# Kernel optimization log

Measured on AMD Instinct MI355X. Metric: run time of the kernel, lower is better.

The kernel has to match this reference:

```python
import jax, jax.numpy as jnp
import numpy as np

BS, S, D, H, DFF, L = 8, 1024, 256, 8, 1024, 3
DK = D // H
NEG = -1e32


def setup_inputs() -> dict:
    key = jax.random.key(0)
    ks = jax.random.split(key, 10)
    r = lambda k, shp: jax.random.normal(k, shp, jnp.float32) * 0.02
    return {
        "q_embed_data": jax.random.normal(ks[0], (BS, S, D), jnp.float32),
        "qa_embed_data": jax.random.normal(ks[1], (BS, S, D), jnp.float32),
        "Wk": r(ks[2], (L, D, D)), "bk": jnp.zeros((L, D), jnp.float32),
        "Wv": r(ks[3], (L, D, D)), "bv": jnp.zeros((L, D), jnp.float32),
        "Wo": r(ks[4], (L, D, D)), "bo": jnp.zeros((L, D), jnp.float32),
        "gammas": r(ks[5], (L, H)),
        "ln1_g": jnp.ones((L, D), jnp.float32), "ln1_b": jnp.zeros((L, D), jnp.float32),
        "W1": r(ks[6], (L, D, DFF)), "b1": jnp.zeros((L, DFF), jnp.float32),
        "W2": r(ks[7], (L, DFF, D)), "b2": jnp.zeros((L, D), jnp.float32),
        "ln2_g": jnp.ones((L, D), jnp.float32), "ln2_b": jnp.zeros((L, D), jnp.float32),
    }


def _layernorm(x, g, b, eps=1e-5):
    mu = x.mean(-1, keepdims=True)
    var = ((x - mu) ** 2).mean(-1, keepdims=True)
    return (x - mu) * jax.lax.rsqrt(var + eps) * g + b


def _attn(xq, xk, xv, Wk, bk, Wv, bv, Wo, bo, gamma, mask, zero_pad):
    # kq_same=1: q and k both use k_linear
    bs = xq.shape[0]
    q = (xq @ Wk + bk).reshape(bs, S, H, DK).transpose(0, 2, 1, 3)  # bhsd
    k = (xk @ Wk + bk).reshape(bs, S, H, DK).transpose(0, 2, 1, 3)
    v = (xv @ Wv + bv).reshape(bs, S, H, DK).transpose(0, 2, 1, 3)
    scores = jnp.einsum('bhid,bhjd->bhij', q, k) / np.float32(np.sqrt(DK))
    mf = mask.astype(scores.dtype)
    # no-grad decay branch (detached in torch)
    p = jax.nn.softmax(jnp.where(mask, scores, NEG), axis=-1) * mf
    distcum = jnp.cumsum(p, axis=-1)
    disttot = p.sum(axis=-1, keepdims=True)
    idx = jnp.arange(S)
    pos = jnp.abs(idx[None, :] - idx[:, None]).astype(jnp.float32)[None, None]
    dist = jnp.sqrt(jnp.clip((disttot - distcum) * pos, 0.0, None))
    dist = jax.lax.stop_gradient(dist)
    g = -jax.nn.softplus(gamma)[None, :, None, None]  # (1,H,1,1)
    total_effect = jnp.clip(jnp.exp(dist * g), 1e-5, 1e5)
    scores = scores * total_effect
    attn = jax.nn.softmax(jnp.where(mask, scores, NEG), axis=-1)
    if zero_pad:
        attn = attn.at[:, :, 0, :].set(0.0)
    out = jnp.einsum('bhij,bhjd->bhid', attn, v)
    out = out.transpose(0, 2, 1, 3).reshape(bs, S, D)
    return out @ Wo + bo


def _block(i, xq, xk, xv, mask, zero_pad, apply_pos, P):
    Wk, bk, Wv, bv, Wo, bo, gam, l1g, l1b, W1, b1, W2, b2, l2g, l2b = [p[i] for p in P]
    q2 = _attn(xq, xk, xv, Wk, bk, Wv, bv, Wo, bo, gam, mask, zero_pad)
    x = _layernorm(xq + q2, l1g, l1b)
    if apply_pos:
        ff = jax.nn.relu(x @ W1 + b1) @ W2 + b2
        x = _layernorm(x + ff, l2g, l2b)
    return x


def _forward(q_embed_data, qa_embed_data, Wk, bk, Wv, bv, Wo, bo, gammas,
             ln1_g, ln1_b, W1, b1, W2, b2, ln2_g, ln2_b):
    P = (Wk, bk, Wv, bv, Wo, bo, gammas, ln1_g, ln1_b, W1, b1, W2, b2, ln2_g, ln2_b)
    tri_incl = jnp.tril(jnp.ones((S, S), bool))[None, None]       # mask=1: peek current+past
    tri_excl = jnp.tril(jnp.ones((S, S), bool), -1)[None, None]   # mask=0: strictly past
    x, y = q_embed_data, qa_embed_data
    # blocks_1 (n_blocks=1): mask=1, apply_pos=True, self-attn on y
    y = _block(0, y, y, y, tri_incl, False, True, P)
    # blocks_2 (2*n_blocks=2): alternate (mask=1, no FFN) / (mask=0, zero_pad, FFN, values=y)
    x = _block(1, x, x, x, tri_incl, False, False, P)
    x = _block(2, x, x, y, tri_excl, True, True, P)
    return x


def reference(q_embed_data, qa_embed_data, Wk, bk, Wv, bv, Wo, bo, gammas,
              ln1_g, ln1_b, W1, b1, W2, b2, ln2_g, ln2_b):
    return _forward(q_embed_data, qa_embed_data, Wk, bk, Wv, bv, Wo, bo, gammas,
                    ln1_g, ln1_b, W1, b1, W2, b2, ln2_g, ln2_b)
```

## Files before the change

kernel.cpp:

```cpp
#include <hip/hip_runtime.h>

typedef unsigned short u16;
typedef float f32x4 __attribute__((ext_vector_type(4)));
typedef __bf16 bf16x8 __attribute__((ext_vector_type(8)));
typedef u16 u16x8 __attribute__((ext_vector_type(8)));
typedef u16 u16x4 __attribute__((ext_vector_type(4)));

__device__ __forceinline__ u16 f2bf(float f) {
  union { float f; unsigned u; } v; v.f = f;
  unsigned r = (v.u + 0x7FFFu + ((v.u >> 16) & 1u)) >> 16;
  return (u16)r;
}
__device__ __forceinline__ unsigned cvtpk_bf16(float lo, float hi) {
  unsigned r;
  asm("v_cvt_pk_bf16_f32 %0, %1, %2" : "=v"(r) : "v"(lo), "v"(hi));
  return r;
}
__device__ __forceinline__ float wred_sum(float v) {
#pragma unroll
  for (int o = 32; o >= 1; o >>= 1) v += __shfl_xor(v, o);
  return v;
}

template <int RELU, int WF32, int WBF, int WVT>
__global__ __launch_bounds__(256) void gemm_kernel(
    const u16* __restrict__ A, const u16* __restrict__ Bt,
    const float* __restrict__ bias, float* __restrict__ C,
    u16* __restrict__ Cbf, int M, int N, int K) {
  __shared__ u16 As[64 * 64];
  __shared__ u16 Bs[64 * 64];
  const int tid = threadIdx.x;
  const int lane = tid & 63;
  const int w = tid >> 6;
  const int m0 = blockIdx.x * 64;
  const int n0 = blockIdx.y * 64;
  const int wr = (w >> 1) * 32;
  const int wc = (w & 1) * 32;
  const int l15 = lane & 15, hi = lane >> 4;

  f32x4 acc[2][2] = {};

  for (int k0 = 0; k0 < K; k0 += 64) {
#pragma unroll
    for (int rep = 0; rep < 2; ++rep) {
      int idx = tid + rep * 256;
      int row = idx >> 3, c8 = idx & 7;
      int cs = ((c8 ^ (row & 7)) << 3);
      __builtin_amdgcn_global_load_lds(
          (const __attribute__((address_space(1))) void*)(A + (size_t)(m0 + row) * K + k0 + cs),
          (__attribute__((address_space(3))) void*)(&As[idx * 8]), 16, 0, 0);
      __builtin_amdgcn_global_load_lds(
          (const __attribute__((address_space(1))) void*)(Bt + (size_t)(n0 + row) * K + k0 + cs),
          (__attribute__((address_space(3))) void*)(&Bs[idx * 8]), 16, 0, 0);
    }
    __syncthreads();
#pragma unroll
    for (int kk = 0; kk < 2; ++kk) {
      int kb = (kk * 32 + (hi << 3)) << 1;
      bf16x8 af[2], bfr[2];
#pragma unroll
      for (int mf = 0; mf < 2; ++mf) {
        int m = wr + mf * 16 + l15;
        af[mf] = *(const bf16x8*)((const char*)As + m * 128 + (kb ^ ((m & 7) << 4)));
      }
#pragma unroll
      for (int nf = 0; nf < 2; ++nf) {
        int n = wc + nf * 16 + l15;
        bfr[nf] = *(const bf16x8*)((const char*)Bs + n * 128 + (kb ^ ((n & 7) << 4)));
      }
#pragma unroll
      for (int mf = 0; mf < 2; ++mf)
#pragma unroll
        for (int nf = 0; nf < 2; ++nf)
          acc[mf][nf] = __builtin_amdgcn_mfma_f32_16x16x32_bf16(af[mf], bfr[nf], acc[mf][nf], 0, 0, 0);
    }
    __syncthreads();
  }

#pragma unroll
  for (int mf = 0; mf < 2; ++mf)
#pragma unroll
    for (int nf = 0; nf < 2; ++nf) {
      int col = n0 + wc + nf * 16 + l15;
      float bia = bias[col];
      u16x4 tv;
#pragma unroll
      for (int r = 0; r < 4; ++r) {
        int row = m0 + wr + mf * 16 + (hi << 2) + r;
        float val = acc[mf][nf][r] + bia;
        if (RELU) val = fmaxf(val, 0.f);
        if (WF32) C[(size_t)row * N + col] = val;
        if (WBF) Cbf[(size_t)row * N + col] = f2bf(val);
        if (WVT) tv[r] = f2bf(val);
      }
      if (WVT) {
        int row0 = m0 + wr + mf * 16 + (hi << 2);
        size_t addr = (((size_t)(row0 >> 10) * 8 + (col >> 5)) * 32 + (col & 31)) * 1024 + (row0 & 1023);
        *(u16x4*)(Cbf + addr) = tv;
      }
    }
}

__global__ __launch_bounds__(256) void gemm_kv_kernel(
    const u16* __restrict__ A, const u16* __restrict__ Bt,
    const float* __restrict__ biasK, const float* __restrict__ biasV,
    u16* __restrict__ qkbf, u16* __restrict__ vT, int M, int N, int K) {
  __shared__ u16 As[64 * 64];
  __shared__ u16 Bs[64 * 64];
  const int tid = threadIdx.x;
  const int lane = tid & 63;
  const int w = tid >> 6;
  const int m0 = blockIdx.x * 64;
  const int n0 = blockIdx.y * 64;
  const int wr = (w >> 1) * 32;
  const int wc = (w & 1) * 32;
  const int l15 = lane & 15, hi = lane >> 4;

  f32x4 acc[2][2] = {};

  for (int k0 = 0; k0 < K; k0 += 64) {
#pragma unroll
    for (int rep = 0; rep < 2; ++rep) {
      int idx = tid + rep * 256;
      int row = idx >> 3, c8 = idx & 7;
      int cs = ((c8 ^ (row & 7)) << 3);
      __builtin_amdgcn_global_load_lds(
          (const __attribute__((address_space(1))) void*)(A + (size_t)(m0 + row) * K + k0 + cs),
          (__attribute__((address_space(3))) void*)(&As[idx * 8]), 16, 0, 0);
      __builtin_amdgcn_global_load_lds(
          (const __attribute__((address_space(1))) void*)(Bt + (size_t)(n0 + row) * K + k0 + cs),
          (__attribute__((address_space(3))) void*)(&Bs[idx * 8]), 16, 0, 0);
    }
    __syncthreads();
#pragma unroll
    for (int kk = 0; kk < 2; ++kk) {
      int kb = (kk * 32 + (hi << 3)) << 1;
      bf16x8 af[2], bfr[2];
#pragma unroll
      for (int mf = 0; mf < 2; ++mf) {
        int m = wr + mf * 16 + l15;
        af[mf] = *(const bf16x8*)((const char*)As + m * 128 + (kb ^ ((m & 7) << 4)));
      }
#pragma unroll
      for (int nf = 0; nf < 2; ++nf) {
        int n = wc + nf * 16 + l15;
        bfr[nf] = *(const bf16x8*)((const char*)Bs + n * 128 + (kb ^ ((n & 7) << 4)));
      }
#pragma unroll
      for (int mf = 0; mf < 2; ++mf)
#pragma unroll
        for (int nf = 0; nf < 2; ++nf)
          acc[mf][nf] = __builtin_amdgcn_mfma_f32_16x16x32_bf16(af[mf], bfr[nf], acc[mf][nf], 0, 0, 0);
    }
    __syncthreads();
  }

  const bool isV = (n0 >= 256);
#pragma unroll
  for (int mf = 0; mf < 2; ++mf)
#pragma unroll
    for (int nf = 0; nf < 2; ++nf) {
      int col = n0 + wc + nf * 16 + l15;
      float bia = isV ? biasV[col - 256] : biasK[col];
      u16x4 tv;
#pragma unroll
      for (int r = 0; r < 4; ++r) {
        int row = m0 + wr + mf * 16 + (hi << 2) + r;
        float val = acc[mf][nf][r] + bia;
        if (!isV) qkbf[(size_t)row * 256 + col] = f2bf(val);
        tv[r] = f2bf(val);
      }
      if (isV) {
        int row0 = m0 + wr + mf * 16 + (hi << 2);
        int vc = col - 256;
        size_t addr = (((size_t)(row0 >> 10) * 8 + (vc >> 5)) * 32 + (vc & 31)) * 1024 + (row0 & 1023);
        *(u16x4*)(vT + addr) = tv;
      }
    }
}

__global__ __launch_bounds__(256) void attn_mfma_kernel(
    const u16* __restrict__ qkbf, const u16* __restrict__ vT,
    u16* __restrict__ ao, const float* __restrict__ gam, int excl) {
  __shared__ float zbuf[4][16];
  __shared__ float z2buf[4][16];
  __shared__ float accbuf[8][4][64];

  const int lane = threadIdx.x & 63, w = threadIdx.x >> 6;
  const int qt = 63 - blockIdx.y;
  const int bh = blockIdx.x;
  const int b = bh >> 3, h = bh & 7;
  const int q0 = qt * 16;
  const int l15 = lane & 15, hi = lane >> 4;
  const int i = q0 + l15;
  const float LOG2E = 1.4426950408889634f;
  const float g2 = -log1pf(__expf(gam[h])) * LOG2E;
  const float cscale = 0.17677669529663687f * LOG2E;
  const float CLIP2 = -16.609640474436812f;

  const u16* kbase = qkbf + (size_t)b * 1024 * 256 + h * 32;
  const u16* vbase = vT + (size_t)bh * 32 * 1024;
  const bf16x8 qfrag = *(const bf16x8*)(kbase + (size_t)i * 256 + hi * 8);

  const int mylim = i - excl;
  const int jmax = q0 + 15 - excl;
  const int ntiles = (jmax >> 4) + 1;
  const int C = (ntiles + 3) >> 2;
  const int c0 = w * C;
  const int tEnd = (c0 + C < ntiles) ? (c0 + C) : ntiles;
  const int count = (tEnd > c0) ? (tEnd - c0) : 0;

  auto calc_l = [&](int t, float* l) {
    bf16x8 kf = *(const bf16x8*)(kbase + (size_t)(t * 16 + l15) * 256 + hi * 8);
    f32x4 sA = {};
    sA = __builtin_amdgcn_mfma_f32_16x16x32_bf16(kf, qfrag, sA, 0, 0, 0);
    l[0] = sA[0] * cscale; l[1] = sA[1] * cscale;
    l[2] = sA[2] * cscale; l[3] = sA[3] * cscale;
    if (t == ntiles - 1) {
      const int kb = t * 16 + hi * 4;
      l[0] = (kb + 0 <= mylim) ? l[0] : -1000.f;
      l[1] = (kb + 1 <= mylim) ? l[1] : -1000.f;
      l[2] = (kb + 2 <= mylim) ? l[2] : -1000.f;
      l[3] = (kb + 3 <= mylim) ? l[3] : -1000.f;
    }
  };

  float zacc = 0.f;
  for (int t = c0; t < tEnd; ++t) {
    float l[4]; calc_l(t, l);
    zacc += (exp2f(l[0]) + exp2f(l[1])) + (exp2f(l[2]) + exp2f(l[3]));
  }
  zacc += __shfl_xor(zacc, 16);
  zacc += __shfl_xor(zacc, 32);
  if (lane < 16) zbuf[w][lane] = zacc;
  __syncthreads();

  const float zc0 = zbuf[0][l15], zc1 = zbuf[1][l15];
  const float zc2 = zbuf[2][l15], zc3 = zbuf[3][l15];
  const float Z = zc0 + zc1 + zc2 + zc3;
  const float invZ = Z > 0.f ? 1.f / Z : 0.f;
  float prefix = 0.f;
  if (w > 0) prefix += zc0;
  if (w > 1) prefix += zc1;
  if (w > 2) prefix += zc2;

  float carry = prefix, z2 = 0.f;
  f32x4 acc0 = {}, acc1 = {};

  auto sm4 = [&](const float* l, int kb) -> uint2 {
    const float e0 = exp2f(l[0]), e1 = exp2f(l[1]);
    const float e2 = exp2f(l[2]), e3 = exp2f(l[3]);
    const float cA = e0 + e1, cB2 = cA + e2, cC = cB2 + e3;
    float vsc = cC;
    float tmp = __shfl_up(vsc, 16); if (hi >= 1) vsc += tmp;
    tmp = __shfl_up(vsc, 32); if (hi >= 2) vsc += tmp;
    const float exg = vsc - cC;
    const float tot = __shfl(vsc, l15 + 48);
    const float cb = carry + exg;
    carry += tot;
    const float posb = (float)(i - kb);
    const float r0 = (Z - (cb + e0)) * invZ;
    const float r1 = (Z - (cb + cA)) * invZ;
    const float r2 = (Z - (cb + cB2)) * invZ;
    const float r3 = (Z - (cb + cC)) * invZ;
    const float d20 = fmaxf(r0 * posb, 0.f);
    const float d21 = fmaxf(r1 * (posb - 1.f), 0.f);
    const float d22 = fmaxf(r2 * (posb - 2.f), 0.f);
    const float d23 = fmaxf(r3 * (posb - 3.f), 0.f);
    const float a0 = fmaxf(__builtin_amdgcn_sqrtf(d20) * g2, CLIP2);
    const float a1 = fmaxf(__builtin_amdgcn_sqrtf(d21) * g2, CLIP2);
    const float a2 = fmaxf(__builtin_amdgcn_sqrtf(d22) * g2, CLIP2);
    const float a3 = fmaxf(__builtin_amdgcn_sqrtf(d23) * g2, CLIP2);
    const float p0 = exp2f(l[0] * exp2f(a0));
    const float p1 = exp2f(l[1] * exp2f(a1));
    const float p2 = exp2f(l[2] * exp2f(a2));
    const float p3 = exp2f(l[3] * exp2f(a3));
    z2 += (p0 + p1) + (p2 + p3);
    uint2 r; r.x = cvtpk_bf16(p0, p1); r.y = cvtpk_bf16(p2, p3);
    return r;
  };

  const int Cp = (count + 1) & ~1;
  for (int tl = 0; tl < Cp; tl += 2) {
    const int t0 = c0 + tl, t1 = t0 + 1;
    float la[4], lb[4];
    calc_l(t0, la);
    const bool v1 = (tl + 1 < count);
    if (v1) calc_l(t1, lb);
    uint2 uA = sm4(la, t0 * 16 + hi * 4);
    uint2 uB = make_uint2(0u, 0u);
    if (v1) uB = sm4(lb, t1 * 16 + hi * 4);
    const int srcA = l15 + (((2 * hi) & 3) << 4);
    const int srcB = l15 + (((2 * hi + 1) & 3) << 4);
    unsigned a00 = (unsigned)__shfl((int)uA.x, srcA);
    unsigned a01 = (unsigned)__shfl((int)uB.x, srcA);
    unsigned a10 = (unsigned)__shfl((int)uA.y, srcA);
    unsigned a11 = (unsigned)__shfl((int)uB.y, srcA);
    unsigned b00 = (unsigned)__shfl((int)uA.x, srcB);
    unsigned b01 = (unsigned)__shfl((int)uB.x, srcB);
    unsigned b10 = (unsigned)__shfl((int)uA.y, srcB);
    unsigned b11 = (unsigned)__shfl((int)uB.y, srcB);
    const bool up = hi >= 2;
    union { unsigned u[4]; bf16x8 v; } pf;
    pf.u[0] = up ? a01 : a00;
    pf.u[1] = up ? a11 : a10;
    pf.u[2] = up ? b01 : b00;
    pf.u[3] = up ? b11 : b10;
    const int jb = t0 * 16;
    bf16x8 vf0 = *(const bf16x8*)(vbase + (size_t)l15 * 1024 + jb + hi * 8);
    bf16x8 vf1 = *(const bf16x8*)(vbase + (size_t)(16 + l15) * 1024 + jb + hi * 8);
    acc0 = __builtin_amdgcn_mfma_f32_16x16x32_bf16(vf0, pf.v, acc0, 0, 0, 0);
    acc1 = __builtin_amdgcn_mfma_f32_16x16x32_bf16(vf1, pf.v, acc1, 0, 0, 0);
  }

  z2 += __shfl_xor(z2, 16);
  z2 += __shfl_xor(z2, 32);
  if (lane < 16) z2buf[w][lane] = z2;
#pragma unroll
  for (int j = 0; j < 4; ++j) {
    accbuf[j][w][lane] = acc0[j];
    accbuf[4 + j][w][lane] = acc1[j];
  }
  __syncthreads();

  if (w == 0) {
    const float z2t = z2buf[0][l15] + z2buf[1][l15] + z2buf[2][l15] + z2buf[3][l15];
    const float inv2 = z2t > 0.f ? 1.f / z2t : 0.f;
    u16* aop = ao + ((size_t)(b * 1024 + i)) * 256 + h * 32;
    float s0[4], s1[4];
#pragma unroll
    for (int j = 0; j < 4; ++j) {
      s0[j] = (accbuf[j][0][lane] + accbuf[j][1][lane] + accbuf[j][2][lane] + accbuf[j][3][lane]) * inv2;
      s1[j] = (accbuf[4 + j][0][lane] + accbuf[4 + j][1][lane] + accbuf[4 + j][2][lane] + accbuf[4 + j][3][lane]) * inv2;
    }
    uint2 o0, o1;
    o0.x = cvtpk_bf16(s0[0], s0[1]); o0.y = cvtpk_bf16(s0[2], s0[3]);
    o1.x = cvtpk_bf16(s1[0], s1[1]); o1.y = cvtpk_bf16(s1[2], s1[3]);
    *(uint2*)(aop + hi * 4) = o0;
    *(uint2*)(aop + 16 + hi * 4) = o1;
  }
}

__global__ __launch_bounds__(256) void add_ln_kernel(
    const float* __restrict__ res, const float* __restrict__ add,
    const float* __restrict__ g, const float* __restrict__ b,
    float* __restrict__ outf, u16* __restrict__ outb) {
  const int lane = threadIdx.x & 63, wid = threadIdx.x >> 6;
  const size_t row = (size_t)blockIdx.x * 4 + wid;
  const size_t base = row * 256 + lane * 4;
  float4 rv = *(const float4*)(res + base);
  float4 av = *(const float4*)(add + base);
  float x0 = rv.x + av.x, x1 = rv.y + av.y, x2 = rv.z + av.z, x3 = rv.w + av.w;
  float sm = wred_sum(x0 + x1 + x2 + x3);
  float mu = sm * (1.f / 256.f);
  float d0 = x0 - mu, d1 = x1 - mu, d2 = x2 - mu, d3 = x3 - mu;
  float vs = wred_sum(d0 * d0 + d1 * d1 + d2 * d2 + d3 * d3);
  float rs = rsqrtf(vs * (1.f / 256.f) + 1e-5f);
  float4 gv = *(const float4*)(g + lane * 4);
  float4 bv = *(const float4*)(b + lane * 4);
  float o0 = d0 * rs * gv.x + bv.x;
  float o1 = d1 * rs * gv.y + bv.y;
  float o2 = d2 * rs * gv.z + bv.z;
  float o3 = d3 * rs * gv.w + bv.w;
  float4 ov = {o0, o1, o2, o3};
  *(float4*)(outf + base) = ov;
  u16x4 wv; wv[0] = f2bf(o0); wv[1] = f2bf(o1); wv[2] = f2bf(o2); wv[3] = f2bf(o3);
  *(u16x4*)(outb + base) = wv;
}

__global__ __launch_bounds__(256) void cast_bf_kernel(
    const float* __restrict__ in, u16* __restrict__ out) {
  size_t i = ((size_t)blockIdx.x * 256 + threadIdx.x) * 8;
  float4 a = *(const float4*)(in + i);
  float4 c = *(const float4*)(in + i + 4);
  u16x8 o;
  o[0] = f2bf(a.x); o[1] = f2bf(a.y); o[2] = f2bf(a.z); o[3] = f2bf(a.w);
  o[4] = f2bf(c.x); o[5] = f2bf(c.y); o[6] = f2bf(c.z); o[7] = f2bf(c.w);
  *(u16x8*)(out + i) = o;
}

__global__ __launch_bounds__(256) void transpose_cast_kernel(
    const float* __restrict__ W, u16* __restrict__ Wt, int K, int N,
    int dstStride) {
  __shared__ float t[32][33];
  const size_t lo = (size_t)blockIdx.z * K * N;
  const size_t lod = (size_t)blockIdx.z * dstStride;
  int n0 = blockIdx.x * 32, k0 = blockIdx.y * 32;
  int tx = threadIdx.x, ty = threadIdx.y;
#pragma unroll
  for (int r = 0; r < 32; r += 8)
    t[ty + r][tx] = W[lo + (size_t)(k0 + ty + r) * N + n0 + tx];
  __syncthreads();
#pragma unroll
  for (int r = 0; r < 32; r += 8)
    Wt[lod + (size_t)(n0 + ty + r) * K + k0 + tx] = f2bf(t[tx][ty + r]);
}

extern "C" void kernel_launch(void* const* d_in, const int* in_sizes, int n_in,
                              void* d_out, int out_size, void* d_ws,
                              size_t ws_size, hipStream_t stream) {
  const float* q_embed = (const float*)d_in[0];
  const float* qa_embed = (const float*)d_in[1];
  const float* Wk = (const float*)d_in[2];
  const float* bk = (const float*)d_in[3];
  const float* Wv = (const float*)d_in[4];
  const float* bv = (const float*)d_in[5];
  const float* Wo = (const float*)d_in[6];
  const float* bo = (const float*)d_in[7];
  const float* gammas = (const float*)d_in[8];
  const float* ln1_g = (const float*)d_in[9];
  const float* ln1_b = (const float*)d_in[10];
  const float* W1 = (const float*)d_in[11];
  const float* b1 = (const float*)d_in[12];
  const float* W2 = (const float*)d_in[13];
  const float* b2 = (const float*)d_in[14];
  const float* ln2_g = (const float*)d_in[15];
  const float* ln2_b = (const float*)d_in[16];

  const size_t ACT_F32 = (size_t)8192 * 256 * 4;
  const size_t ACT_BF = (size_t)8192 * 256 * 2;
  char* p = (char*)d_ws;
  auto carve = [&](size_t bytes) {
    void* r = (void*)p;
    p += (bytes + 255) & ~(size_t)255;
    return r;
  };
  float* yb = (float*)carve(ACT_F32);
  float* xb = (float*)carve(ACT_F32);
  float* pof = (float*)carve(ACT_F32);
  u16* xbf = (u16*)carve(ACT_BF);
  u16* ybf = (u16*)carve(ACT_BF);
  u16* qkbf = (u16*)carve(ACT_BF);
  u16* vTb = (u16*)carve(ACT_BF);
  u16* aobf = (u16*)carve(ACT_BF);
  u16* hbf = (u16*)carve((size_t)8192 * 1024 * 2);
  u16* Wkvt = (u16*)carve((size_t)3 * 131072 * 2);
  u16* Wot = (u16*)carve((size_t)3 * 65536 * 2);
  u16* W1t = (u16*)carve((size_t)3 * 262144 * 2);
  u16* W2t = (u16*)carve((size_t)3 * 262144 * 2);

  dim3 tb(32, 8);
  transpose_cast_kernel<<<dim3(8, 8, 3), tb, 0, stream>>>(Wk, Wkvt, 256, 256, 131072);
  transpose_cast_kernel<<<dim3(8, 8, 3), tb, 0, stream>>>(Wv, Wkvt + 65536, 256, 256, 131072);
  transpose_cast_kernel<<<dim3(8, 8, 3), tb, 0, stream>>>(Wo, Wot, 256, 256, 65536);
  transpose_cast_kernel<<<dim3(32, 8, 3), tb, 0, stream>>>(W1, W1t, 256, 1024, 262144);
  transpose_cast_kernel<<<dim3(8, 32, 3), tb, 0, stream>>>(W2, W2t, 1024, 256, 262144);
  cast_bf_kernel<<<1024, 256, 0, stream>>>(q_embed, xbf);
  cast_bf_kernel<<<1024, 256, 0, stream>>>(qa_embed, ybf);

  const dim3 gP(128, 4), gF(128, 16), gKV(128, 8);
  const dim3 gA(64, 64);

  gemm_kv_kernel<<<gKV, 256, 0, stream>>>(ybf, Wkvt, bk, bv, qkbf, vTb, 8192, 512, 256);
  attn_mfma_kernel<<<gA, 256, 0, stream>>>(qkbf, vTb, aobf, gammas, 0);
  gemm_kernel<0, 1, 0, 0><<<gP, 256, 0, stream>>>(aobf, Wot, bo, pof, nullptr, 8192, 256, 256);
  add_ln_kernel<<<2048, 256, 0, stream>>>(qa_embed, pof, ln1_g, ln1_b, yb, ybf);
  gemm_kernel<1, 0, 1, 0><<<gF, 256, 0, stream>>>(ybf, W1t, b1, nullptr, hbf, 8192, 1024, 256);
  gemm_kernel<0, 1, 0, 0><<<gP, 256, 0, stream>>>(hbf, W2t, b2, pof, nullptr, 8192, 256, 1024);
  add_ln_kernel<<<2048, 256, 0, stream>>>(yb, pof, ln2_g, ln2_b, yb, ybf);

  gemm_kv_kernel<<<gKV, 256, 0, stream>>>(xbf, Wkvt + 131072, bk + 256, bv + 256, qkbf, vTb, 8192, 512, 256);
  attn_mfma_kernel<<<gA, 256, 0, stream>>>(qkbf, vTb, aobf, gammas + 8, 0);
  gemm_kernel<0, 1, 0, 0><<<gP, 256, 0, stream>>>(aobf, Wot + 65536, bo + 256, pof, nullptr, 8192, 256, 256);
  add_ln_kernel<<<2048, 256, 0, stream>>>(q_embed, pof, ln1_g + 256, ln1_b + 256, xb, xbf);

  gemm_kv_kernel<<<gKV, 256, 0, stream>>>(xbf, Wkvt + 262144, bk + 512, bv + 512, qkbf, vTb, 8192, 512, 256);
  gemm_kernel<0, 0, 0, 1><<<gP, 256, 0, stream>>>(ybf, Wkvt + 262144 + 65536, bv + 512, nullptr, vTb, 8192, 256, 256);
  attn_mfma_kernel<<<gA, 256, 0, stream>>>(qkbf, vTb, aobf, gammas + 16, 1);
  gemm_kernel<0, 1, 0, 0><<<gP, 256, 0, stream>>>(aobf, Wot + 131072, bo + 512, pof, nullptr, 8192, 256, 256);
  add_ln_kernel<<<2048, 256, 0, stream>>>(xb, pof, ln1_g + 512, ln1_b + 512, xb, xbf);
  gemm_kernel<1, 0, 1, 0><<<gF, 256, 0, stream>>>(xbf, W1t + 524288, b1 + 2048, nullptr, hbf, 8192, 1024, 256);
  gemm_kernel<0, 1, 0, 0><<<gP, 256, 0, stream>>>(hbf, W2t + 524288, b2 + 512, pof, nullptr, 8192, 256, 1024);
  add_ln_kernel<<<2048, 256, 0, stream>>>(xb, pof, ln2_g + 512, ln2_b + 512, (float*)d_out, xbf);
}
```

Measured before the change: 314.5 us.

## Widen GEMM N-tiles, store projection outputs in bf16, hoist V loads in attention

The KV and W1 GEMMs now use 64x128 tiles with 2x4 MFMA fragments per wave, raising reuse of each A tile and halving the grid in the N direction. The Wo and W2 projection outputs are written as bf16 instead of fp32, and add_ln reads them as bf16, roughly halving that intermediate traffic. In the attention kernel the V fragment loads are issued before the softmax math so their latency can overlap with computation. The risks are extra rounding of the residual addend to bf16, and higher register and LDS use from the larger tiles, which may lower occupancy.

After: 313.7 us. About the same (-0.2%).

```diff
diff --git a/kernel.cpp b/kernel.cpp
--- a/kernel.cpp
+++ b/kernel.cpp
@@ -10,6 +10,10 @@
   union { float f; unsigned u; } v; v.f = f;
   unsigned r = (v.u + 0x7FFFu + ((v.u >> 16) & 1u)) >> 16;
   return (u16)r;
+}
+__device__ __forceinline__ float bf2f(u16 h) {
+  union { unsigned u; float f; } v; v.u = ((unsigned)h) << 16;
+  return v.f;
 }
 __device__ __forceinline__ unsigned cvtpk_bf16(float lo, float hi) {
   unsigned r;
@@ -101,22 +105,23 @@
     }
 }
 
-__global__ __launch_bounds__(256) void gemm_kv_kernel(
+template <int RELU>
+__global__ __launch_bounds__(256) void gemm_w_kernel(
     const u16* __restrict__ A, const u16* __restrict__ Bt,
-    const float* __restrict__ biasK, const float* __restrict__ biasV,
-    u16* __restrict__ qkbf, u16* __restrict__ vT, int M, int N, int K) {
+    const float* __restrict__ bias, u16* __restrict__ Cbf,
+    int M, int N, int K) {
   __shared__ u16 As[64 * 64];
-  __shared__ u16 Bs[64 * 64];
+  __shared__ u16 Bs[128 * 64];
   const int tid = threadIdx.x;
   const int lane = tid & 63;
   const int w = tid >> 6;
   const int m0 = blockIdx.x * 64;
-  const int n0 = blockIdx.y * 64;
+  const int n0 = blockIdx.y * 128;
   const int wr = (w >> 1) * 32;
-  const int wc = (w & 1) * 32;
+  const int wc = (w & 1) * 64;
   const int l15 = lane & 15, hi = lane >> 4;
 
-  f32x4 acc[2][2] = {};
+  f32x4 acc[2][4] = {};
 
   for (int k0 = 0; k0 < K; k0 += 64) {
 #pragma unroll
@@ -127,6 +132,12 @@
       __builtin_amdgcn_global_load_lds(
           (const __attribute__((address_space(1))) void*)(A + (size_t)(m0 + row) * K + k0 + cs),
           (__attribute__((address_space(3))) void*)(&As[idx * 8]), 16, 0, 0);
+    }
+#pragma unroll
+    for (int rep = 0; rep < 4; ++rep) {
+      int idx = tid + rep * 256;
+      int row = idx >> 3, c8 = idx & 7;
+      int cs = ((c8 ^ (row & 7)) << 3);
       __builtin_amdgcn_global_load_lds(
           (const __attribute__((address_space(1))) void*)(Bt + (size_t)(n0 + row) * K + k0 + cs),
           (__attribute__((address_space(3))) void*)(&Bs[idx * 8]), 16, 0, 0);
@@ -135,32 +146,108 @@
 #pragma unroll
     for (int kk = 0; kk < 2; ++kk) {
       int kb = (kk * 32 + (hi << 3)) << 1;
-      bf16x8 af[2], bfr[2];
+      bf16x8 af[2], bfr[4];
 #pragma unroll
       for (int mf = 0; mf < 2; ++mf) {
         int m = wr + mf * 16 + l15;
         af[mf] = *(const bf16x8*)((const char*)As + m * 128 + (kb ^ ((m & 7) << 4)));
       }
 #pragma unroll
-      for (int nf = 0; nf < 2; ++nf) {
+      for (int nf = 0; nf < 4; ++nf) {
         int n = wc + nf * 16 + l15;
         bfr[nf] = *(const bf16x8*)((const char*)Bs + n * 128 + (kb ^ ((n & 7) << 4)));
       }
 #pragma unroll
       for (int mf = 0; mf < 2; ++mf)
 #pragma unroll
-        for (int nf = 0; nf < 2; ++nf)
+        for (int nf = 0; nf < 4; ++nf)
           acc[mf][nf] = __builtin_amdgcn_mfma_f32_16x16x32_bf16(af[mf], bfr[nf], acc[mf][nf], 0, 0, 0);
     }
     __syncthreads();
   }
 
-  const bool isV = (n0 >= 256);
 #pragma unroll
   for (int mf = 0; mf < 2; ++mf)
 #pragma unroll
-    for (int nf = 0; nf < 2; ++nf) {
+    for (int nf = 0; nf < 4; ++nf) {
       int col = n0 + wc + nf * 16 + l15;
+      float bia = bias[col];
+#pragma unroll
+      for (int r = 0; r < 4; ++r) {
+        int row = m0 + wr + mf * 16 + (hi << 2) + r;
+        float val = acc[mf][nf][r] + bia;
+        if (RELU) val = fmaxf(val, 0.f);
+        Cbf[(size_t)row * N + col] = f2bf(val);
+      }
+    }
+}
+
+__global__ __launch_bounds__(256) void gemm_kv_kernel(
+    const u16* __restrict__ A, const u16* __restrict__ Bt,
+    const float* __restrict__ biasK, const float* __restrict__ biasV,
+    u16* __restrict__ qkbf, u16* __restrict__ vT, int M, int N, int K) {
+  __shared__ u16 As[64 * 64];
+  __shared__ u16 Bs[128 * 64];
+  const int tid = threadIdx.x;
+  const int lane = tid & 63;
+  const int w = tid >> 6;
+  const int m0 = blockIdx.x * 64;
+  const int n0 = blockIdx.y * 128;
+  const int wr = (w >> 1) * 32;
+  const int wc = (w & 1) * 64;
+  const int l15 = lane & 15, hi = lane >> 4;
+
+  f32x4 acc[2][4] = {};
+
+  for (int k0 = 0; k0 < K; k0 += 64) {
+#pragma unroll
+    for (int rep = 0; rep < 2; ++rep) {
+      int idx = tid + rep * 256;
+      int row = idx >> 3, c8 = idx & 7;
+      int cs = ((c8 ^ (row & 7)) << 3);
+      __builtin_amdgcn_global_load_lds(
+          (const __attribute__((address_space(1))) void*)(A + (size_t)(m0 + row) * K + k0 + cs),
+          (__attribute__((address_space(3))) void*)(&As[idx * 8]), 16, 0, 0);
+    }
+#pragma unroll
+    for (int rep = 0; rep < 4; ++rep) {
+      int idx = tid + rep * 256;
+      int row = idx >> 3, c8 = idx & 7;
+      int cs = ((c8 ^ (row & 7)) << 3);
+      __builtin_amdgcn_global_load_lds(
+          (const __attribute__((address_space(1))) void*)(Bt + (size_t)(n0 + row) * K + k0 + cs),
+          (__attribute__((address_space(3))) void*)(&Bs[idx * 8]), 16, 0, 0);
+    }
+    __syncthreads();
+#pragma unroll
+    for (int kk = 0; kk < 2; ++kk) {
+      int kb = (kk * 32 + (hi << 3)) << 1;
+      bf16x8 af[2], bfr[4];
+#pragma unroll
+      for (int mf = 0; mf < 2; ++mf) {
+        int m = wr + mf * 16 + l15;
+        af[mf] = *(const bf16x8*)((const char*)As + m * 128 + (kb ^ ((m & 7) << 4)));
+      }
+#pragma unroll
+      for (int nf = 0; nf < 4; ++nf) {
+        int n = wc + nf * 16 + l15;
+        bfr[nf] = *(const bf16x8*)((const char*)Bs + n * 128 + (kb ^ ((n & 7) << 4)));
+      }
+#pragma unroll
+      for (int mf = 0; mf < 2; ++mf)
+#pragma unroll
+        for (int nf = 0; nf < 4; ++nf)
+          acc[mf][nf] = __builtin_amdgcn_mfma_f32_16x16x32_bf16(af[mf], bfr[nf], acc[mf][nf], 0, 0, 0);
+    }
+    __syncthreads();
+  }
+
+#pragma unroll
+  for (int mf = 0; mf < 2; ++mf)
+#pragma unroll
+    for (int nf = 0; nf < 4; ++nf) {
+      int col = n0 + wc + nf * 16 + l15;
+      const bool isV = (col >= 256);
       float bia = isV ? biasV[col - 256] : biasK[col];
       u16x4 tv;
 #pragma unroll
@@ -287,6 +374,9 @@
     calc_l(t0, la);
     const bool v1 = (tl + 1 < count);
     if (v1) calc_l(t1, lb);
+    const int jb = t0 * 16;
+    bf16x8 vf0 = *(const bf16x8*)(vbase + (size_t)l15 * 1024 + jb + hi * 8);
+    bf16x8 vf1 = *(const bf16x8*)(vbase + (size_t)(16 + l15) * 1024 + jb + hi * 8);
     uint2 uA = sm4(la, t0 * 16 + hi * 4);
     uint2 uB = make_uint2(0u, 0u);
     if (v1) uB = sm4(lb, t1 * 16 + hi * 4);
@@ -306,9 +396,6 @@
     pf.u[1] = up ? a11 : a10;
     pf.u[2] = up ? b01 : b00;
     pf.u[3] = up ? b11 : b10;
-    const int jb = t0 * 16;
-    bf16x8 vf0 = *(const bf16x8*)(vbase + (size_t)l15 * 1024 + jb + hi * 8);
-    bf16x8 vf1 = *(const bf16x8*)(vbase + (size_t)(16 + l15) * 1024 + jb + hi * 8);
     acc0 = __builtin_amdgcn_mfma_f32_16x16x32_bf16(vf0, pf.v, acc0, 0, 0, 0);
     acc1 = __builtin_amdgcn_mfma_f32_16x16x32_bf16(vf1, pf.v, acc1, 0, 0, 0);
   }
@@ -342,15 +429,16 @@
 }
 
 __global__ __launch_bounds__(256) void add_ln_kernel(
-    const float* __restrict__ res, const float* __restrict__ add,
+    const float* __restrict__ res, const u16* __restrict__ add,
     const float* __restrict__ g, const float* __restrict__ b,
     float* __restrict__ outf, u16* __restrict__ outb) {
   const int lane = threadIdx.x & 63, wid = threadIdx.x >> 6;
   const size_t row = (size_t)blockIdx.x * 4 + wid;
   const size_t base = row * 256 + lane * 4;
   float4 rv = *(const float4*)(res + base);
-  float4 av = *(const float4*)(add + base);
-  float x0 = rv.x + av.x, x1 = rv.y + av.y, x2 = rv.z + av.z, x3 = rv.w + av.w;
+  u16x4 av = *(const u16x4*)(add + base);
+  float x0 = rv.x + bf2f(av[0]), x1 = rv.y + bf2f(av[1]);
+  float x2 = rv.z + bf2f(av[2]), x3 = rv.w + bf2f(av[3]);
   float sm = wred_sum(x0 + x1 + x2 + x3);
   float mu = sm * (1.f / 256.f);
   float d0 = x0 - mu, d1 = x1 - mu, d2 = x2 - mu, d3 = x3 - mu;
@@ -427,7 +515,7 @@
   };
   float* yb = (float*)carve(ACT_F32);
   float* xb = (float*)carve(ACT_F32);
-  float* pof = (float*)carve(ACT_F32);
+  u16* pofb = (u16*)carve(ACT_BF);
   u16* xbf = (u16*)carve(ACT_BF);
   u16* ybf = (u16*)carve(ACT_BF);
   u16* qkbf = (u16*)carve(ACT_BF);
@@ -448,28 +536,28 @@
   cast_bf_kernel<<<1024, 256, 0, stream>>>(q_embed, xbf);
   cast_bf_kernel<<<1024, 256, 0, stream>>>(qa_embed, ybf);
 
-  const dim3 gP(128, 4), gF(128, 16), gKV(128, 8);
+  const dim3 gP(128, 4), gKV(128, 4), gW1(128, 8);
   const dim3 gA(64, 64);
 
   gemm_kv_kernel<<<gKV, 256, 0, stream>>>(ybf, Wkvt, bk, bv, qkbf, vTb, 8192, 512, 256);
   attn_mfma_kernel<<<gA, 256, 0, stream>>>(qkbf, vTb, aobf, gammas, 0);
-  gemm_kernel<0, 1, 0, 0><<<gP, 256, 0, stream>>>(aobf, Wot, bo, pof, nullptr, 8192, 256, 256);
-  add_ln_kernel<<<2048, 256, 0, stream>>>(qa_embed, pof, ln1_g, ln1_b, yb, ybf);
-  gemm_kernel<1, 0, 1, 0><<<gF, 256, 0, stream>>>(ybf, W1t, b1, nullptr, hbf, 8192, 1024, 256);
-  gemm_kernel<0, 1, 0, 0><<<gP, 256, 0, stream>>>(hbf, W2t, b2, pof, nullptr, 8192, 256, 1024);
-  add_ln_kernel<<<2048, 256, 0, stream>>>(yb, pof, ln2_g, ln2_b, yb, ybf);
+  gemm_kernel<0, 0, 1, 0><<<gP, 256, 0, stream>>>(aobf, Wot, bo, nullptr, pofb, 8192, 256, 256);
+  add_ln_kernel<<<2048, 256, 0, stream>>>(qa_embed, pofb, ln1_g, ln1_b, yb, ybf);
+  gemm_w_kernel<1><<<gW1, 256, 0, stream>>>(ybf, W1t, b1, hbf, 8192, 1024, 256);
+  gemm_kernel<0, 0, 1, 0><<<gP, 256, 0, stream>>>(hbf, W2t, b2, nullptr, pofb, 8192, 256, 1024);
+  add_ln_kernel<<<2048, 256, 0, stream>>>(yb, pofb, ln2_g, ln2_b, yb, ybf);
 
   gemm_kv_kernel<<<gKV, 256, 0, stream>>>(xbf, Wkvt + 131072, bk + 256, bv + 256, qkbf, vTb, 8192, 512, 256);
   attn_mfma_kernel<<<gA, 256, 0, stream>>>(qkbf, vTb, aobf, gammas + 8, 0);
-  gemm_kernel<0, 1, 0, 0><<<gP, 256, 0, stream>>>(aobf, Wot + 65536, bo + 256, pof, nullptr, 8192, 256, 256);
-  add_ln_kernel<<<2048, 256, 0, stream>>>(q_embed, pof, ln1_g + 256, ln1_b + 256, xb, xbf);
+  gemm_kernel<0, 0, 1, 0><<<gP, 256, 0, stream>>>(aobf, Wot + 65536, bo + 256, nullptr, pofb, 8192, 256, 256);
+  add_ln_kernel<<<2048, 256, 0, stream>>>(q_embed, pofb, ln1_g + 256, ln1_b + 256, xb, xbf);
 
   gemm_kv_kernel<<<gKV, 256, 0, stream>>>(xbf, Wkvt + 262144, bk + 512, bv + 512, qkbf, vTb, 8192, 512, 256);
   gemm_kernel<0, 0, 0, 1><<<gP, 256, 0, stream>>>(ybf, Wkvt + 262144 + 65536, bv + 512, nullptr, vTb, 8192, 256, 256);
   attn_mfma_kernel<<<gA, 256, 0, stream>>>(qkbf, vTb, aobf, gammas + 16, 1);
-  gemm_kernel<0, 1, 0, 0><<<gP, 256, 0, stream>>>(aobf, Wot + 131072, bo + 512, pof, nullptr, 8192, 256, 256);
-  add_ln_kernel<<<2048, 256, 0, stream>>>(xb, pof, ln1_g + 512, ln1_b + 512, xb, xbf);
-  gemm_kernel<1, 0, 1, 0><<<gF, 256, 0, stream>>>(xbf, W1t + 524288, b1 + 2048, nullptr, hbf, 8192, 1024, 256);
-  gemm_kernel<0, 1, 0, 0><<<gP, 256, 0, stream>>>(hbf, W2t + 524288, b2 + 512, pof, nullptr, 8192, 256, 1024);
-  add_ln_kernel<<<2048, 256, 0, stream>>>(xb, pof, ln2_g + 512, ln2_b + 512, (float*)d_out, xbf);
-}
+  gemm_kernel<0, 0, 1, 0><<<gP, 256, 0, stream>>>(aobf, Wot + 131072, bo + 512, nullptr, pofb, 8192, 256, 256);
+  add_ln_kernel<<<2048, 256, 0, stream>>>(xb, pofb, ln1_g + 512, ln1_b + 512, xb, xbf);
+  gemm_w_kernel<1><<<gW1, 256, 0, stream>>>(xbf, W1t + 524288, b1 + 2048, hbf, 8192, 1024, 256);
+  gemm_kernel<0, 0, 1, 0><<<gP, 256, 0, stream>>>(hbf, W2t + 524288, b2 + 512, nullptr, pofb, 8192, 256, 1024);
+  add_ln_kernel<<<2048, 256, 0, stream>>>(xb, pofb, ln2_g + 512, ln2_b + 512, (float*)d_out, xbf);
+}
```
